# Kernel tuning notes

Hardware: AMD Instinct MI355X
Metric: run time of the kernel (lower is better)

## Reference

```python
import jax, jax.numpy as jnp
import numpy as np

B, S, D, H, E, N = 4, 1024, 1024, 4096, 1024, 8


def setup_inputs() -> dict:
    key = jax.random.key(0)
    ks = jax.random.split(key, 5)
    x = jax.random.normal(ks[0], (B, S, D), jnp.float32)
    # Learned parameters (Linear weights stored as [in, out] for x @ W)
    Wg = jax.random.normal(ks[1], (D, N), jnp.float32) * 0.02
    bg = jnp.zeros((N,), jnp.float32)
    W1 = jax.random.normal(ks[2], (N, D, H), jnp.float32) * 0.02
    b1 = jnp.zeros((N, H), jnp.float32)
    W2 = jax.random.normal(ks[3], (N, H, E), jnp.float32) * 0.02
    b2 = jnp.zeros((N, E), jnp.float32)
    return {"x": x, "Wg": Wg, "bg": bg, "W1": W1, "b1": b1,
            "W2": W2, "b2": b2, "num_experts_per_tok": 2}


def reference(x, Wg, bg, W1, b1, W2, b2, num_experts_per_tok):
    # Gating: softmax over experts
    gate_probs = jax.nn.softmax(x @ Wg + bg, axis=-1)            # [B,S,N]
    n_exp = gate_probs.shape[-1]
    # Top-k routing mask (indices are distinct, so summed one-hots == scatter of 1.0)
    _, topk_idx = jax.lax.top_k(gate_probs, num_experts_per_tok)  # [B,S,k]
    mask = jax.nn.one_hot(topk_idx, n_exp, dtype=gate_probs.dtype).sum(axis=-2)  # [B,S,N]
    gated = gate_probs * mask
    # F.normalize(p=1): divide by max(L1-norm, eps)
    gated = gated / jnp.maximum(jnp.sum(jnp.abs(gated), axis=-1, keepdims=True), 1e-12)
    # Dense all-expert FFN (matches torch.stack over ModuleList)
    h = jax.nn.relu(jnp.einsum('bsd,ndh->bsnh', x, W1) + b1)      # [B,S,N,H]
    expert_out = jnp.einsum('bsnh,nhe->bsne', h, W2) + b2          # [B,S,N,E]
    out = jnp.einsum('bsn,bsne->bse', gated, expert_out)           # [B,S,E]
    # Auxiliary load-balancing stats
    tokens = float(x.shape[0] * x.shape[1])
    importance = gate_probs.sum(axis=(0, 1)) / tokens              # [N]
    load = mask.sum(axis=(0, 1)) / tokens                          # [N]
    lb_loss = (n_exp * (importance * load).sum()).astype(out.dtype)
    return out, lb_loss, importance, load
```

## Files before the change

kernel.cpp:

```cpp
#include <hip/hip_runtime.h>

#define TOKENS 4096
#define DDIM 1024
#define HDIM 4096
#define EDIM 1024
#define NEXP 8
#define SLOTS (TOKENS * 2)
#define OUT_MAIN ((size_t)TOKENS * EDIM)

typedef __bf16 bf16_t;
typedef bf16_t bf16x8 __attribute__((ext_vector_type(8)));
typedef float f32x4 __attribute__((ext_vector_type(4)));

__device__ __forceinline__ unsigned short f32_to_bf16(float f) {
  union { float f; unsigned u; } v; v.f = f;
  unsigned r = v.u + 0x7FFFu + ((v.u >> 16) & 1u);
  return (unsigned short)(r >> 16);
}

__device__ __forceinline__ void gload_lds16(const void* g, void* l) {
  __builtin_amdgcn_global_load_lds(
      (__attribute__((address_space(1))) void*)(g),
      (__attribute__((address_space(3))) void*)(l), 16, 0, 0);
}

__global__ __launch_bounds__(256) void gate_kernel(
    const float* __restrict__ x, const float* __restrict__ Wg,
    const float* __restrict__ bg, unsigned short* __restrict__ xb,
    int2* __restrict__ tok_e, float2* __restrict__ tok_w,
    float* __restrict__ probs) {
  const int wave = threadIdx.x >> 6;
  const int lane = threadIdx.x & 63;
  const int t = blockIdx.x * 4 + wave;
  const float4* xr = reinterpret_cast<const float4*>(x + (size_t)t * DDIM);
  ushort4* xbr = reinterpret_cast<ushort4*>(xb + (size_t)t * DDIM);

  float acc[NEXP];
#pragma unroll
  for (int n = 0; n < NEXP; n++) acc[n] = 0.f;

#pragma unroll
  for (int i = 0; i < 4; i++) {
    int d4 = lane + 64 * i;
    float4 xv = xr[d4];
    ushort4 o;
    o.x = f32_to_bf16(xv.x); o.y = f32_to_bf16(xv.y);
    o.z = f32_to_bf16(xv.z); o.w = f32_to_bf16(xv.w);
    xbr[d4] = o;
    const float* wrow = Wg + (size_t)d4 * 4 * NEXP;
#pragma unroll
    for (int n = 0; n < NEXP; n++)
      acc[n] += xv.x * wrow[n] + xv.y * wrow[NEXP + n] +
                xv.z * wrow[2 * NEXP + n] + xv.w * wrow[3 * NEXP + n];
  }
#pragma unroll
  for (int n = 0; n < NEXP; n++)
#pragma unroll
    for (int m = 32; m > 0; m >>= 1) acc[n] += __shfl_xor(acc[n], m, 64);

  if (lane == 0) {
    float p[NEXP];
    float mx = -1e30f;
#pragma unroll
    for (int n = 0; n < NEXP; n++) { p[n] = acc[n] + bg[n]; mx = fmaxf(mx, p[n]); }
    float s = 0.f;
#pragma unroll
    for (int n = 0; n < NEXP; n++) { p[n] = expf(p[n] - mx); s += p[n]; }
    float inv = 1.f / s;
#pragma unroll
    for (int n = 0; n < NEXP; n++) { p[n] *= inv; probs[(size_t)t * NEXP + n] = p[n]; }
    int e1 = 0; float p1 = p[0];
#pragma unroll
    for (int n = 1; n < NEXP; n++) if (p[n] > p1) { p1 = p[n]; e1 = n; }
    int e2 = (e1 == 0) ? 1 : 0; float p2 = p[e2];
#pragma unroll
    for (int n = 0; n < NEXP; n++) if (n != e1 && p[n] > p2) { p2 = p[n]; e2 = n; }
    float denom = p1 + p2;
    tok_e[t] = make_int2(e1, e2);
    tok_w[t] = make_float2(p1 / denom, p2 / denom);
  }
}

__global__ __launch_bounds__(1024) void route_kernel(
    const int2* __restrict__ tok_e, const float2* __restrict__ tok_w,
    int* __restrict__ offs_g, int* __restrict__ counts_g,
    int* __restrict__ token_ids, float* __restrict__ slot_w) {
  __shared__ int cnt[NEXP];
  __shared__ int offs[NEXP + 1];
  __shared__ int cur[NEXP];
  const int tid = threadIdx.x;
  if (tid < NEXP) cnt[tid] = 0;
  __syncthreads();
  int2 e[4]; float2 w[4];
#pragma unroll
  for (int i = 0; i < 4; i++) {
    int t = tid + 1024 * i;
    e[i] = tok_e[t]; w[i] = tok_w[t];
    atomicAdd(&cnt[e[i].x], 1);
    atomicAdd(&cnt[e[i].y], 1);
  }
  __syncthreads();
  if (tid == 0) {
    int s = 0;
#pragma unroll
    for (int n = 0; n < NEXP; n++) { offs[n] = s; cur[n] = s; s += cnt[n]; }
    offs[NEXP] = s;
  }
  __syncthreads();
  if (tid < NEXP) { offs_g[tid] = offs[tid]; counts_g[tid] = cnt[tid]; }
  if (tid == 0) offs_g[NEXP] = offs[NEXP];
#pragma unroll
  for (int i = 0; i < 4; i++) {
    int t = tid + 1024 * i;
    int s0 = atomicAdd(&cur[e[i].x], 1);
    token_ids[s0] = t; slot_w[s0] = w[i].x;
    int s1 = atomicAdd(&cur[e[i].y], 1);
    token_ids[s1] = t; slot_w[s1] = w[i].y;
  }
}

__global__ __launch_bounds__(256) void transpose_convert_kernel(
    const float* __restrict__ src, unsigned short* __restrict__ dst, int R, int C) {
  __shared__ float tile[32][33];
  const size_t mat = (size_t)R * C;
  const float* s = src + (size_t)blockIdx.z * mat;
  unsigned short* d = dst + (size_t)blockIdx.z * mat;
  int c0 = blockIdx.x * 32, r0 = blockIdx.y * 32;
  int tx = threadIdx.x, ty = threadIdx.y;
#pragma unroll
  for (int i = 0; i < 32; i += 8)
    tile[ty + i][tx] = s[(size_t)(r0 + ty + i) * C + (c0 + tx)];
  __syncthreads();
#pragma unroll
  for (int i = 0; i < 32; i += 8)
    d[(size_t)(c0 + ty + i) * R + (r0 + tx)] = f32_to_bf16(tile[tx][ty + i]);
}

__global__ __launch_bounds__(256) void gemm1_kernel(
    const unsigned short* __restrict__ xb, const unsigned short* __restrict__ w1t,
    const float* __restrict__ b1, const int* __restrict__ token_ids,
    const int* __restrict__ offs, unsigned short* __restrict__ h) {
  const int e = blockIdx.z;
  const int off0 = offs[e];
  const int ne = offs[e + 1] - off0;
  const int mt = blockIdx.y;
  if (mt * 128 >= ne) return;
  const int nt = blockIdx.x;

  __shared__ unsigned short As[128 * 64];
  __shared__ unsigned short Bs[128 * 64];

  const int tid = threadIdx.x;
  const int lane = tid & 63;
  const int wave = tid >> 6;
  const int wm = (wave >> 1) * 64;
  const int wn = (wave & 1) * 64;

  const int prow = tid >> 3;
  const int krow = (tid & 7) ^ (prow & 7);
  const unsigned short* gA[4];
  const unsigned short* gB[4];
  const unsigned short* wbase = w1t + (size_t)e * HDIM * DDIM;
#pragma unroll
  for (int j = 0; j < 4; j++) {
    int row = prow + j * 32;
    int slot = off0 + min(mt * 128 + row, ne - 1);
    gA[j] = xb + (size_t)token_ids[slot] * DDIM + krow * 8;
    gB[j] = wbase + (size_t)(nt * 128 + row) * DDIM + krow * 8;
  }

  f32x4 acc[4][4];
#pragma unroll
  for (int i = 0; i < 4; i++)
#pragma unroll
    for (int j = 0; j < 4; j++) acc[i][j] = (f32x4)(0.f);

  const int frow = lane & 15;
  const int q = lane >> 4;

  for (int k0 = 0; k0 < DDIM; k0 += 64) {
    __syncthreads();
#pragma unroll
    for (int j = 0; j < 4; j++) {
      gload_lds16(gA[j] + k0, As + j * 2048 + wave * 512);
      gload_lds16(gB[j] + k0, Bs + j * 2048 + wave * 512);
    }
    __syncthreads();
#pragma unroll
    for (int kk = 0; kk < 2; kk++) {
      bf16x8 af[4], bfv[4];
#pragma unroll
      for (int mi = 0; mi < 4; mi++) {
        int row = wm + mi * 16 + frow;
        int k16 = (kk * 4 + q) ^ (row & 7);
        af[mi] = *reinterpret_cast<const bf16x8*>(&As[row * 64 + k16 * 8]);
      }
#pragma unroll
      for (int ni = 0; ni < 4; ni++) {
        int row = wn + ni * 16 + frow;
        int k16 = (kk * 4 + q) ^ (row & 7);
        bfv[ni] = *reinterpret_cast<const bf16x8*>(&Bs[row * 64 + k16 * 8]);
      }
#pragma unroll
      for (int mi = 0; mi < 4; mi++)
#pragma unroll
        for (int ni = 0; ni < 4; ni++)
          acc[mi][ni] = __builtin_amdgcn_mfma_f32_16x16x32_bf16(af[mi], bfv[ni], acc[mi][ni], 0, 0, 0);
    }
  }

  const float* b1e = b1 + (size_t)e * HDIM + nt * 128;
  const int r4 = (lane >> 4) * 4;
  const int cb = lane & 15;
#pragma unroll
  for (int mi = 0; mi < 4; mi++) {
#pragma unroll
    for (int r = 0; r < 4; r++) {
      int grow = mt * 128 + wm + mi * 16 + r4 + r;
      if (grow < ne) {
        unsigned short* hr = h + (size_t)(off0 + grow) * HDIM + nt * 128;
#pragma unroll
        for (int ni = 0; ni < 4; ni++) {
          int col = wn + ni * 16 + cb;
          float v = acc[mi][ni][r] + b1e[col];
          hr[col] = f32_to_bf16(fmaxf(v, 0.f));
        }
      }
    }
  }
}

__global__ __launch_bounds__(512) void gemm2_kernel(
    const unsigned short* __restrict__ h, const unsigned short* __restrict__ w2t,
    const float* __restrict__ b2, const int* __restrict__ token_ids,
    const float* __restrict__ slot_w, const int* __restrict__ offs,
    float* __restrict__ out) {
  const int e = blockIdx.z;
  const int off0 = offs[e];
  const int ne = offs[e + 1] - off0;
  const int mt = blockIdx.y;
  if (mt * 128 >= ne) return;
  const int nt = blockIdx.x;

  __shared__ unsigned short As[128 * 64];
  __shared__ unsigned short Bs[256 * 64];

  const int tid = threadIdx.x;
  const int lane = tid & 63;
  const int wave = tid >> 6;
  const int wm = (wave >> 2) * 64;
  const int wn = (wave & 3) * 64;

  const int prow = tid >> 3;
  const int krow = (tid & 7) ^ (prow & 7);
  const unsigned short* gA[2];
  const unsigned short* gB[4];
  const unsigned short* wbase = w2t + (size_t)e * EDIM * HDIM;
#pragma unroll
  for (int j = 0; j < 2; j++) {
    int row = prow + j * 64;
    int slot = off0 + min(mt * 128 + row, ne - 1);
    gA[j] = h + (size_t)slot * HDIM + krow * 8;
  }
#pragma unroll
  for (int j = 0; j < 4; j++) {
    int row = prow + j * 64;
    gB[j] = wbase + (size_t)(nt * 256 + row) * HDIM + krow * 8;
  }

  f32x4 acc[4][4];
#pragma unroll
  for (int i = 0; i < 4; i++)
#pragma unroll
    for (int j = 0; j < 4; j++) acc[i][j] = (f32x4)(0.f);

  const int frow = lane & 15;
  const int q = lane >> 4;

  for (int k0 = 0; k0 < HDIM; k0 += 64) {
    __syncthreads();
#pragma unroll
    for (int j = 0; j < 2; j++)
      gload_lds16(gA[j] + k0, As + j * 4096 + wave * 512);
#pragma unroll
    for (int j = 0; j < 4; j++)
      gload_lds16(gB[j] + k0, Bs + j * 4096 + wave * 512);
    __syncthreads();
#pragma unroll
    for (int kk = 0; kk < 2; kk++) {
      bf16x8 af[4], bfv[4];
#pragma unroll
      for (int mi = 0; mi < 4; mi++) {
        int row = wm + mi * 16 + frow;
        int k16 = (kk * 4 + q) ^ (row & 7);
        af[mi] = *reinterpret_cast<const bf16x8*>(&As[row * 64 + k16 * 8]);
      }
#pragma unroll
      for (int ni = 0; ni < 4; ni++) {
        int row = wn + ni * 16 + frow;
        int k16 = (kk * 4 + q) ^ (row & 7);
        bfv[ni] = *reinterpret_cast<const bf16x8*>(&Bs[row * 64 + k16 * 8]);
      }
#pragma unroll
      for (int mi = 0; mi < 4; mi++)
#pragma unroll
        for (int ni = 0; ni < 4; ni++)
          acc[mi][ni] = __builtin_amdgcn_mfma_f32_16x16x32_bf16(af[mi], bfv[ni], acc[mi][ni], 0, 0, 0);
    }
  }

  const float* b2e = b2 + (size_t)e * EDIM + nt * 256;
  const int r4 = (lane >> 4) * 4;
  const int cb = lane & 15;
#pragma unroll
  for (int mi = 0; mi < 4; mi++) {
#pragma unroll
    for (int r = 0; r < 4; r++) {
      int grow = mt * 128 + wm + mi * 16 + r4 + r;
      if (grow < ne) {
        int slot = off0 + grow;
        int tokid = token_ids[slot];
        float wgt = slot_w[slot];
        float* orow = out + (size_t)tokid * EDIM + nt * 256;
#pragma unroll
        for (int ni = 0; ni < 4; ni++) {
          int col = wn + ni * 16 + cb;
          float v = (acc[mi][ni][r] + b2e[col]) * wgt;
          atomicAdd(&orow[col], v);
        }
      }
    }
  }
}

__global__ __launch_bounds__(512) void stats_kernel(
    const float* __restrict__ probs, const int* __restrict__ counts,
    float* __restrict__ tail) {
  const int wave = threadIdx.x >> 6;
  const int lane = threadIdx.x & 63;
  float s = 0.f;
  for (int t = lane; t < TOKENS; t += 64) s += probs[(size_t)t * NEXP + wave];
#pragma unroll
  for (int m = 32; m > 0; m >>= 1) s += __shfl_xor(s, m, 64);
  __shared__ float imp_s[NEXP];
  if (lane == 0) imp_s[wave] = s / (float)TOKENS;
  __syncthreads();
  if (threadIdx.x == 0) {
    float lb = 0.f;
#pragma unroll
    for (int n = 0; n < NEXP; n++) {
      float imp = imp_s[n];
      float ld = (float)counts[n] / (float)TOKENS;
      tail[1 + n] = imp;
      tail[1 + NEXP + n] = ld;
      lb += imp * ld;
    }
    tail[0] = (float)NEXP * lb;
  }
}

extern "C" void kernel_launch(void* const* d_in, const int* in_sizes, int n_in,
                              void* d_out, int out_size, void* d_ws, size_t ws_size,
                              hipStream_t stream) {
  const float* x  = (const float*)d_in[0];
  const float* Wg = (const float*)d_in[1];
  const float* bg = (const float*)d_in[2];
  const float* W1 = (const float*)d_in[3];
  const float* b1 = (const float*)d_in[4];
  const float* W2 = (const float*)d_in[5];
  const float* b2 = (const float*)d_in[6];
  float* out = (float*)d_out;
  char* ws = (char*)d_ws;

  const size_t XB_OFF   = 0;
  const size_t W1T_OFF  = XB_OFF + (size_t)TOKENS * DDIM * 2;
  const size_t W2T_OFF  = W1T_OFF + (size_t)NEXP * DDIM * HDIM * 2;
  const size_t H_OFF    = W2T_OFF + (size_t)NEXP * HDIM * EDIM * 2;
  const size_t TOKE_OFF = H_OFF + (size_t)SLOTS * HDIM * 2;
  const size_t TOKW_OFF = TOKE_OFF + (size_t)TOKENS * sizeof(int2);
  const size_t TID_OFF  = TOKW_OFF + (size_t)TOKENS * sizeof(float2);
  const size_t SLW_OFF  = TID_OFF + (size_t)SLOTS * 4;
  const size_t PROB_OFF = SLW_OFF + (size_t)SLOTS * 4;
  const size_t META_OFF = PROB_OFF + (size_t)TOKENS * NEXP * 4;
  const size_t WS_NEED  = META_OFF + 64 * 4;
  if (ws_size < WS_NEED) return;

  unsigned short* xb   = (unsigned short*)(ws + XB_OFF);
  unsigned short* w1t  = (unsigned short*)(ws + W1T_OFF);
  unsigned short* w2t  = (unsigned short*)(ws + W2T_OFF);
  unsigned short* hbuf = (unsigned short*)(ws + H_OFF);
  int2*   tok_e = (int2*)(ws + TOKE_OFF);
  float2* tok_w = (float2*)(ws + TOKW_OFF);
  int*    tids  = (int*)(ws + TID_OFF);
  float*  slw   = (float*)(ws + SLW_OFF);
  float*  probs = (float*)(ws + PROB_OFF);
  int*    counts = (int*)(ws + META_OFF);
  int*    offs   = counts + 8;

  hipMemsetAsync(out, 0, (size_t)out_size * sizeof(float), stream);

  gate_kernel<<<TOKENS / 4, 256, 0, stream>>>(x, Wg, bg, xb, tok_e, tok_w, probs);
  route_kernel<<<1, 1024, 0, stream>>>(tok_e, tok_w, offs, counts, tids, slw);
  transpose_convert_kernel<<<dim3(HDIM / 32, DDIM / 32, NEXP), dim3(32, 8), 0, stream>>>(W1, w1t, DDIM, HDIM);
  transpose_convert_kernel<<<dim3(EDIM / 32, HDIM / 32, NEXP), dim3(32, 8), 0, stream>>>(W2, w2t, HDIM, EDIM);
  gemm1_kernel<<<dim3(HDIM / 128, SLOTS / 128, NEXP), 256, 0, stream>>>(xb, w1t, b1, tids, offs, hbuf);
  gemm2_kernel<<<dim3(EDIM / 256, SLOTS / 128, NEXP), 512, 0, stream>>>(hbuf, w2t, b2, tids, slw, offs, out);
  stats_kernel<<<1, 512, 0, stream>>>(probs, counts, out + OUT_MAIN);
}
```

Measured before the change: 486.5 us.

## Split-K the second expert GEMM and widen the weight transpose-convert tiles

The second grouped GEMM now uses 128x128 tiles with 256 threads and splits the hidden dimension into two K chunks, each on its own block. Both chunks atomically add into the output, and only the first chunk adds the bias. The aim is more blocks to fill the GPU, at the cost of twice the atomic traffic to the output. The weight transpose/convert kernel also moves to 64x64 tiles with float4 loads and ushort4 stores, to cut memory transactions on the conversion of W1 and W2.

```diff
diff --git a/kernel.cpp b/kernel.cpp
--- a/kernel.cpp
+++ b/kernel.cpp
@@ -7,6 +7,8 @@
 #define NEXP 8
 #define SLOTS (TOKENS * 2)
 #define OUT_MAIN ((size_t)TOKENS * EDIM)
+#define NKC2 2
+#define KCHUNK2 (HDIM / NKC2)
 
 typedef __bf16 bf16_t;
 typedef bf16_t bf16x8 __attribute__((ext_vector_type(8)));
@@ -121,19 +123,32 @@
 
 __global__ __launch_bounds__(256) void transpose_convert_kernel(
     const float* __restrict__ src, unsigned short* __restrict__ dst, int R, int C) {
-  __shared__ float tile[32][33];
+  __shared__ float tile[64][65];
   const size_t mat = (size_t)R * C;
   const float* s = src + (size_t)blockIdx.z * mat;
   unsigned short* d = dst + (size_t)blockIdx.z * mat;
-  int c0 = blockIdx.x * 32, r0 = blockIdx.y * 32;
-  int tx = threadIdx.x, ty = threadIdx.y;
-#pragma unroll
-  for (int i = 0; i < 32; i += 8)
-    tile[ty + i][tx] = s[(size_t)(r0 + ty + i) * C + (c0 + tx)];
+  int c0 = blockIdx.x * 64, r0 = blockIdx.y * 64;
+  int tx = threadIdx.x & 15, ty = threadIdx.x >> 4;
+#pragma unroll
+  for (int i = 0; i < 4; i++) {
+    int row = ty + 16 * i;
+    float4 v = *reinterpret_cast<const float4*>(&s[(size_t)(r0 + row) * C + c0 + tx * 4]);
+    tile[row][tx * 4 + 0] = v.x;
+    tile[row][tx * 4 + 1] = v.y;
+    tile[row][tx * 4 + 2] = v.z;
+    tile[row][tx * 4 + 3] = v.w;
+  }
   __syncthreads();
 #pragma unroll
-  for (int i = 0; i < 32; i += 8)
-    d[(size_t)(c0 + ty + i) * R + (r0 + tx)] = f32_to_bf16(tile[tx][ty + i]);
+  for (int i = 0; i < 4; i++) {
+    int col = ty + 16 * i;
+    ushort4 o;
+    o.x = f32_to_bf16(tile[tx * 4 + 0][col]);
+    o.y = f32_to_bf16(tile[tx * 4 + 1][col]);
+    o.z = f32_to_bf16(tile[tx * 4 + 2][col]);
+    o.w = f32_to_bf16(tile[tx * 4 + 3][col]);
+    *reinterpret_cast<ushort4*>(&d[(size_t)(c0 + col) * R + r0 + tx * 4]) = o;
+  }
 }
 
 __global__ __launch_bounds__(256) void gemm1_kernel(
@@ -230,12 +245,14 @@
   }
 }
 
-__global__ __launch_bounds__(512) void gemm2_kernel(
+__global__ __launch_bounds__(256) void gemm2_kernel(
     const unsigned short* __restrict__ h, const unsigned short* __restrict__ w2t,
     const float* __restrict__ b2, const int* __restrict__ token_ids,
     const float* __restrict__ slot_w, const int* __restrict__ offs,
     float* __restrict__ out) {
-  const int e = blockIdx.z;
+  const int ez = blockIdx.z;
+  const int e = ez >> 1;
+  const int kc = ez & 1;
   const int off0 = offs[e];
   const int ne = offs[e + 1] - off0;
   const int mt = blockIdx.y;
@@ -243,29 +260,25 @@
   const int nt = blockIdx.x;
 
   __shared__ unsigned short As[128 * 64];
-  __shared__ unsigned short Bs[256 * 64];
+  __shared__ unsigned short Bs[128 * 64];
 
   const int tid = threadIdx.x;
   const int lane = tid & 63;
   const int wave = tid >> 6;
-  const int wm = (wave >> 2) * 64;
-  const int wn = (wave & 3) * 64;
+  const int wm = (wave >> 1) * 64;
+  const int wn = (wave & 1) * 64;
 
   const int prow = tid >> 3;
   const int krow = (tid & 7) ^ (prow & 7);
-  const unsigned short* gA[2];
+  const unsigned short* gA[4];
   const unsigned short* gB[4];
   const unsigned short* wbase = w2t + (size_t)e * EDIM * HDIM;
 #pragma unroll
-  for (int j = 0; j < 2; j++) {
-    int row = prow + j * 64;
+  for (int j = 0; j < 4; j++) {
+    int row = prow + j * 32;
     int slot = off0 + min(mt * 128 + row, ne - 1);
     gA[j] = h + (size_t)slot * HDIM + krow * 8;
-  }
-#pragma unroll
-  for (int j = 0; j < 4; j++) {
-    int row = prow + j * 64;
-    gB[j] = wbase + (size_t)(nt * 256 + row) * HDIM + krow * 8;
+    gB[j] = wbase + (size_t)(nt * 128 + row) * HDIM + krow * 8;
   }
 
   f32x4 acc[4][4];
@@ -277,14 +290,13 @@
   const int frow = lane & 15;
   const int q = lane >> 4;
 
-  for (int k0 = 0; k0 < HDIM; k0 += 64) {
+  for (int k0 = kc * KCHUNK2; k0 < (kc + 1) * KCHUNK2; k0 += 64) {
     __syncthreads();
 #pragma unroll
-    for (int j = 0; j < 2; j++)
-      gload_lds16(gA[j] + k0, As + j * 4096 + wave * 512);
-#pragma unroll
-    for (int j = 0; j < 4; j++)
-      gload_lds16(gB[j] + k0, Bs + j * 4096 + wave * 512);
+    for (int j = 0; j < 4; j++) {
+      gload_lds16(gA[j] + k0, As + j * 2048 + wave * 512);
+      gload_lds16(gB[j] + k0, Bs + j * 2048 + wave * 512);
+    }
     __syncthreads();
 #pragma unroll
     for (int kk = 0; kk < 2; kk++) {
@@ -309,7 +321,7 @@
     }
   }
 
-  const float* b2e = b2 + (size_t)e * EDIM + nt * 256;
+  const float* b2e = b2 + (size_t)e * EDIM + nt * 128;
   const int r4 = (lane >> 4) * 4;
   const int cb = lane & 15;
 #pragma unroll
@@ -321,12 +333,12 @@
         int slot = off0 + grow;
         int tokid = token_ids[slot];
         float wgt = slot_w[slot];
-        float* orow = out + (size_t)tokid * EDIM + nt * 256;
+        float* orow = out + (size_t)tokid * EDIM + nt * 128;
 #pragma unroll
         for (int ni = 0; ni < 4; ni++) {
           int col = wn + ni * 16 + cb;
-          float v = (acc[mi][ni][r] + b2e[col]) * wgt;
-          atomicAdd(&orow[col], v);
+          float bias = (kc == 0) ? b2e[col] : 0.f;
+          atomicAdd(&orow[col], (acc[mi][ni][r] + bias) * wgt);
         }
       }
     }
@@ -401,9 +413,9 @@
 
   gate_kernel<<<TOKENS / 4, 256, 0, stream>>>(x, Wg, bg, xb, tok_e, tok_w, probs);
   route_kernel<<<1, 1024, 0, stream>>>(tok_e, tok_w, offs, counts, tids, slw);
-  transpose_convert_kernel<<<dim3(HDIM / 32, DDIM / 32, NEXP), dim3(32, 8), 0, stream>>>(W1, w1t, DDIM, HDIM);
-  transpose_convert_kernel<<<dim3(EDIM / 32, HDIM / 32, NEXP), dim3(32, 8), 0, stream>>>(W2, w2t, HDIM, EDIM);
+  transpose_convert_kernel<<<dim3(HDIM / 64, DDIM / 64, NEXP), 256, 0, stream>>>(W1, w1t, DDIM, HDIM);
+  transpose_convert_kernel<<<dim3(EDIM / 64, HDIM / 64, NEXP), 256, 0, stream>>>(W2, w2t, HDIM, EDIM);
   gemm1_kernel<<<dim3(HDIM / 128, SLOTS / 128, NEXP), 256, 0, stream>>>(xb, w1t, b1, tids, offs, hbuf);
-  gemm2_kernel<<<dim3(EDIM / 256, SLOTS / 128, NEXP), 512, 0, stream>>>(hbuf, w2t, b2, tids, slw, offs, out);
+  gemm2_kernel<<<dim3(EDIM / 128, SLOTS / 128, NEXP * NKC2), 256, 0, stream>>>(hbuf, w2t, b2, tids, slw, offs, out);
   stats_kernel<<<1, 512, 0, stream>>>(probs, counts, out + OUT_MAIN);
 }
```

Result: faster. 473.6 us (-2.7%).
